# Kernel tuning notes

Measured on AMD Instinct MI355X. Metric: run time of the kernel, lower is better.

Reference implementation:

```python
import jax, jax.numpy as jnp
import numpy as np

V, E, H, W, S, T, B = 10000, 256, 512, 256, 512, 128, 64


def setup_inputs() -> dict:
    key = jax.random.key(0)
    ks = jax.random.split(key, 17)
    def rn(k, shape, s=0.08):
        return jax.random.normal(k, shape, jnp.float32) * s
    return {
        "tokens": jax.random.randint(ks[0], (B, S), 0, V),
        "dec_h0": jax.random.normal(ks[1], (B, H), jnp.float32),
        "emb_table": rn(ks[2], (V, E), 1.0),
        "enc_Wih": rn(ks[3], (4 * H, E)),
        "enc_Whh": rn(ks[4], (4 * H, H)),
        "enc_bih": rn(ks[5], (4 * H,)),
        "enc_bhh": rn(ks[6], (4 * H,)),
        "dec_Wih": rn(ks[7], (4 * H, E)),
        "dec_Whh": rn(ks[8], (4 * H, H)),
        "dec_bih": rn(ks[9], (4 * H,)),
        "dec_bhh": rn(ks[10], (4 * H,)),
        "W1_w": rn(ks[11], (W, H)),
        "W1_b": rn(ks[12], (W,)),
        "W2_w": rn(ks[13], (W, H)),
        "W2_b": rn(ks[14], (W,)),
        "vt_w": rn(ks[15], (1, W)),
        "vt_b": rn(ks[16], (1,)),
    }


def _lstm_cell(x, h, c, Wih, Whh, bih, bhh):
    # PyTorch gate order: input, forget, cell(g), output
    gates = x @ Wih.T + h @ Whh.T + bih + bhh
    i, f, g, o = jnp.split(gates, 4, axis=-1)
    c = jax.nn.sigmoid(f) * c + jax.nn.sigmoid(i) * jnp.tanh(g)
    h = jax.nn.sigmoid(o) * jnp.tanh(c)
    return h, c


def reference(tokens, dec_h0, emb_table, enc_Wih, enc_Whh, enc_bih, enc_bhh,
              dec_Wih, dec_Whh, dec_bih, dec_bhh, W1_w, W1_b, W2_w, W2_b,
              vt_w, vt_b):
    emb = emb_table[tokens]                       # [B,S,E]
    x_sbe = jnp.swapaxes(emb, 0, 1)               # [S,B,E] time-major
    bsz = tokens.shape[0]
    h0 = jnp.zeros((bsz, enc_Whh.shape[1]), emb.dtype)

    def enc_step(carry, x):
        h, c = carry
        h, c = _lstm_cell(x, h, c, enc_Wih, enc_Whh, enc_bih, enc_bhh)
        return (h, c), h

    _, enc_states = jax.lax.scan(enc_step, (h0, h0), x_sbe)   # [S,B,H]

    # W1(encoder_states) is constant across decoder steps -> hoist it
    blend1 = enc_states @ W1_w.T + W1_b            # [S,B,W]
    c0 = enc_states[-1]                            # original uses last enc state as cell init
    dec_in = jnp.zeros((bsz, emb_table.shape[1]), emb.dtype)  # never updated in original

    def dec_step(carry, _):
        h, c = carry
        h, c = _lstm_cell(dec_in, h, c, dec_Wih, dec_Whh, dec_bih, dec_bhh)
        blend2 = h @ W2_w.T + W2_b                 # [B,W]
        u = (jnp.tanh(blend1 + blend2[None]) @ vt_w.T)[..., 0] + vt_b[0]  # [S,B]
        logp = jax.nn.log_softmax(u.T, axis=1)     # [B,S], softmax over seq positions
        return (h, c), logp

    _, probs = jax.lax.scan(dec_step, (dec_h0, c0), None, length=T)  # [T,B,S]
    return jnp.swapaxes(probs, 0, 1)               # [B,T,S]
```

## Files before the change

kernel.cpp:

```cpp
#include <hip/hip_runtime.h>
#include <hip/hip_bf16.h>
#include <cstdint>
#include <cstddef>

typedef __bf16 bf16_t;
typedef __bf16 bf16x8 __attribute__((ext_vector_type(8)));
typedef float  f32x4  __attribute__((ext_vector_type(4)));

#define NB 64
#define NS 512
#define NTD 128
#define NE 256
#define NH 512
#define NG 2048
#define NW 256

#define HSTEP_DW 16384u

__device__ __forceinline__ float sigm_f(float x) { return 1.f / (1.f + __expf(-x)); }
__device__ __forceinline__ float tanh_f(float x) {
  float e = __expf(2.f * x);
  return 1.f - 2.f / (e + 1.f);
}
__device__ __forceinline__ float bits2f(uint32_t b16) {
  uint32_t u = b16 << 16;
  return __builtin_bit_cast(float, u);
}
__device__ __forceinline__ uint32_t packh(float a, float b) {
  uint16_t lo = __builtin_bit_cast(uint16_t, (bf16_t)a);
  uint16_t hi = __builtin_bit_cast(uint16_t, (bf16_t)b);
  return (uint32_t)lo | ((uint32_t)hi << 16);
}
__device__ __forceinline__ uint32_t aload(const uint32_t* p) {
  return __hip_atomic_load(p, __ATOMIC_RELAXED, __HIP_MEMORY_SCOPE_AGENT);
}
__device__ __forceinline__ uint64_t aload64(const uint64_t* p) {
  return __hip_atomic_load(p, __ATOMIC_RELAXED, __HIP_MEMORY_SCOPE_AGENT);
}
__device__ __forceinline__ void astore(uint32_t* p, uint32_t v) {
  __hip_atomic_store(p, v, __ATOMIC_RELAXED, __HIP_MEMORY_SCOPE_AGENT);
}

__global__ __launch_bounds__(256) void pack_all(
    const float* __restrict__ s0, bf16_t* __restrict__ d0,
    const float* __restrict__ s1, bf16_t* __restrict__ d1,
    const float* __restrict__ s2, bf16_t* __restrict__ d2,
    const float* __restrict__ s3, bf16_t* __restrict__ d3,
    const float* __restrict__ s4, bf16_t* __restrict__ d4) {
  int blk = blockIdx.x;
  const float* src; bf16_t* dst; int K, idx;
  if (blk < 2048)       { src = s0; dst = d0; K = 256; idx = blk * 256 + threadIdx.x; }
  else if (blk < 6144)  { src = s1; dst = d1; K = 512; idx = (blk - 2048) * 256 + threadIdx.x; }
  else if (blk < 10240) { src = s2; dst = d2; K = 512; idx = (blk - 6144) * 256 + threadIdx.x; }
  else if (blk < 10752) { src = s3; dst = d3; K = 512; idx = (blk - 10240) * 256 + threadIdx.x; }
  else                  { src = s4; dst = d4; K = 512; idx = (blk - 10752) * 256 + threadIdx.x; }
  int n = idx / K, k = idx - n * K;
  int lane = (((k & 31) >> 3) << 4) | (n & 15);
  size_t o = ((((size_t)(n >> 4) * (K >> 5)) + (k >> 5)) * 64 + lane) * 8 + (k & 7);
  dst[o] = (bf16_t)src[idx];
}

__global__ __launch_bounds__(256) void gather_emb2(
    const int* __restrict__ tokens, const float* __restrict__ table,
    bf16_t* __restrict__ embfrag, const float* __restrict__ dec_h0,
    uint32_t* __restrict__ dec_hf0) {
  int blk = blockIdx.x;
  if (blk < 4096) {
    int idx = blk * 256 + threadIdx.x;
    int row = idx >> 5, e0 = (idx & 31) << 3;
    int b = row & 63, s = row >> 6;
    int tok = tokens[b * NS + s];
    const float4* p = (const float4*)(table + (size_t)tok * NE + e0);
    float4 v0 = p[0], v1 = p[1];
    bf16x8 v;
    v[0] = (bf16_t)v0.x; v[1] = (bf16_t)v0.y; v[2] = (bf16_t)v0.z; v[3] = (bf16_t)v0.w;
    v[4] = (bf16_t)v1.x; v[5] = (bf16_t)v1.y; v[6] = (bf16_t)v1.z; v[7] = (bf16_t)v1.w;
    int mt = row >> 4;
    int ks = e0 >> 5;
    int lane = (b & 15) | (((e0 >> 3) & 3) << 4);
    *(bf16x8*)(embfrag + ((size_t)(mt * 8 + ks) * 64 + lane) * 8) = v;
  } else {
    int idx = (blk - 4096) * 256 + threadIdx.x;
    int b = idx >> 8, jp = idx & 255;
    int j = jp * 2;
    float lo = dec_h0[(size_t)b * NH + j], hi = dec_h0[(size_t)b * NH + j + 1];
    int bg = b >> 4, bl = b & 15, ks = j >> 5;
    int lane = bl | (((j >> 3) & 3) << 4);
    dec_hf0[((size_t)bg * 16 + ks) * 256 + lane * 4 + ((j >> 1) & 3)] = packh(lo, hi);
  }
}

__global__ __launch_bounds__(256) void gemm_blends(
    const bf16_t* __restrict__ encA, const bf16_t* __restrict__ W1p,
    const float* __restrict__ W1_b, bf16_t* __restrict__ blend1,
    const bf16_t* __restrict__ decA, const bf16_t* __restrict__ W2p,
    const float* __restrict__ W2_b, float* __restrict__ blend2) {
  union SMU { bf16_t t16[16][68]; float t32[16][68]; };
  __shared__ SMU tile;
  const int KS = 16;
  int lane = threadIdx.x & 63, w = threadIdx.x >> 6;
  int nt = blockIdx.x * 4 + w;
  bool is1 = blockIdx.y < 128;
  int mt0 = (is1 ? blockIdx.y : (blockIdx.y - 128)) * 16;
  const bf16_t* A  = is1 ? encA : decA;
  const bf16_t* Bp = is1 ? W1p : W2p;
  const float* bias = is1 ? W1_b : W2_b;
  bf16x8 bfr[KS];
  const bf16_t* bp = Bp + ((size_t)nt * KS * 64 + lane) * 8;
#pragma unroll
  for (int ks = 0; ks < KS; ++ks) bfr[ks] = *(const bf16x8*)(bp + (size_t)ks * 512);
  int col = (nt << 4) + (lane & 15);
  float bs = bias[col];
  int row0 = (lane >> 4) << 2;
  int rw = threadIdx.x >> 4, ch = threadIdx.x & 15;
  for (int m = 0; m < 16; ++m) {
    int mt = mt0 + m;
    const bf16_t* ap = A + (size_t)mt * (KS * 512) + lane * 8;
    f32x4 acc = {0.f, 0.f, 0.f, 0.f};
#pragma unroll
    for (int ks = 0; ks < KS; ++ks)
      acc = __builtin_amdgcn_mfma_f32_16x16x32_bf16(
          *(const bf16x8*)(ap + (size_t)ks * 512), bfr[ks], acc, 0, 0, 0);
    if (is1) {
#pragma unroll
      for (int r = 0; r < 4; ++r)
        tile.t16[row0 + r][w * 16 + (lane & 15)] = (bf16_t)(acc[r] + bs);
      __syncthreads();
      ushort4 v = *(const ushort4*)&tile.t16[rw][ch * 4];
      *(ushort4*)(blend1 + (size_t)(mt * 16 + rw) * NW + blockIdx.x * 64 + ch * 4) = v;
      __syncthreads();
    } else {
#pragma unroll
      for (int r = 0; r < 4; ++r)
        tile.t32[row0 + r][w * 16 + (lane & 15)] = acc[r] + bs;
      __syncthreads();
      float4 v = *(const float4*)&tile.t32[rw][ch * 4];
      *(float4*)(blend2 + (size_t)(mt * 16 + rw) * NW + blockIdx.x * 64 + ch * 4) = v;
      __syncthreads();
    }
  }
}

__global__ __launch_bounds__(256) void lstm_chain_enc(
    const bf16_t* __restrict__ Wp, const bf16_t* __restrict__ Wihp,
    const bf16_t* __restrict__ embfrag, const float* __restrict__ bih,
    const float* __restrict__ bhh, uint32_t* __restrict__ hfrag,
    uint32_t* __restrict__ flags) {
  __shared__ bf16_t wlds[8 * 8192];
  __shared__ float gl[4][16][36];
  int tid = threadIdx.x, lane = tid & 63, wv = tid >> 6;
  int bg = blockIdx.x >> 4, slice = blockIdx.x & 15;

  for (int l = 0; l < 8; ++l) {
    int g = l >> 1, p = l & 1;
    const bf16_t* src = Wp + (size_t)(g * 32 + slice * 2 + p) * 8192;
    bf16_t* dst = wlds + (size_t)l * 8192;
    for (int i = tid; i < 1024; i += 256)
      *(bf16x8*)(dst + (size_t)i * 8) = *(const bf16x8*)(src + (size_t)i * 8);
  }
  bf16x8 xf0[8], xf1[8];
  {
    int nt0 = wv * 32 + slice * 2;
    const bf16_t* p0 = Wihp + (((size_t)nt0 * 8) * 64 + lane) * 8;
    const bf16_t* p1 = Wihp + (((size_t)(nt0 + 1) * 8) * 64 + lane) * 8;
#pragma unroll
    for (int ks = 0; ks < 8; ++ks) {
      xf0[ks] = *(const bf16x8*)(p0 + (size_t)ks * 512);
      xf1[ks] = *(const bf16x8*)(p1 + (size_t)ks * 512);
    }
  }

  int ub = tid >> 4, uj2 = tid & 15;
  int j_lo = slice * 32 + uj2 * 2;
  int lane_f = ub | ((uj2 >> 2) << 4);
  float c0 = 0.f, c1 = 0.f;
  float bsum[4][2];
#pragma unroll
  for (int g = 0; g < 4; ++g) {
    bsum[g][0] = bih[g * NH + j_lo] + bhh[g * NH + j_lo];
    bsum[g][1] = bih[g * NH + j_lo + 1] + bhh[g * NH + j_lo + 1];
  }
  __syncthreads();

  const uint64_t* hq = (const uint64_t*)hfrag;
  uint32_t* fl = flags + bg * 16;

  for (int t = 0; t < NS; ++t) {
    bf16x8 ea[8];
    const bf16_t* eb = embfrag + (((size_t)(t * 4 + bg) * 8) * 64 + lane) * 8;
#pragma unroll
    for (int ks = 0; ks < 8; ++ks) ea[ks] = *(const bf16x8*)(eb + (size_t)ks * 512);
    if (t > 0) {
      uint32_t tgt = (uint32_t)t;
      bool ok;
      do {
        uint32_t f = tgt;
        if (lane < 16 && lane != (uint32_t)slice) f = aload(fl + lane);
        ok = __all(f >= tgt);
      } while (!ok);
    }
    f32x4 acc0 = {0.f, 0.f, 0.f, 0.f}, acc1 = {0.f, 0.f, 0.f, 0.f};
#pragma unroll
    for (int ks = 0; ks < 8; ++ks) {
      acc0 = __builtin_amdgcn_mfma_f32_16x16x32_bf16(ea[ks], xf0[ks], acc0, 0, 0, 0);
      acc1 = __builtin_amdgcn_mfma_f32_16x16x32_bf16(ea[ks], xf1[ks], acc1, 0, 0, 0);
    }
    const uint64_t* hb = hq + ((size_t)t * 4 + bg) * 2048 + lane * 2;
    uint64_t aq[16][2];
#pragma unroll
    for (int ks = 0; ks < 16; ++ks) {
      aq[ks][0] = aload64(hb + (size_t)ks * 128);
      aq[ks][1] = aload64(hb + (size_t)ks * 128 + 1);
    }
    const bf16_t* wl = wlds + (size_t)(wv * 2) * 8192 + lane * 8;
#pragma unroll
    for (int ks = 0; ks < 16; ++ks) {
      union { uint64_t q[2]; bf16x8 v; } u;
      u.q[0] = aq[ks][0]; u.q[1] = aq[ks][1];
      acc0 = __builtin_amdgcn_mfma_f32_16x16x32_bf16(
          u.v, *(const bf16x8*)(wl + (size_t)ks * 512), acc0, 0, 0, 0);
      acc1 = __builtin_amdgcn_mfma_f32_16x16x32_bf16(
          u.v, *(const bf16x8*)(wl + 8192 + (size_t)ks * 512), acc1, 0, 0, 0);
    }
    int cc = lane & 15, rb = (lane >> 4) << 2;
#pragma unroll
    for (int r = 0; r < 4; ++r) {
      gl[wv][rb + r][cc] = acc0[r];
      gl[wv][rb + r][16 + cc] = acc1[r];
    }
    __syncthreads();

    float p[4][2];
#pragma unroll
    for (int g = 0; g < 4; ++g) {
      p[g][0] = gl[g][ub][uj2 * 2] + bsum[g][0];
      p[g][1] = gl[g][ub][uj2 * 2 + 1] + bsum[g][1];
    }
    float i0 = sigm_f(p[0][0]), f0 = sigm_f(p[1][0]);
    float g0 = tanh_f(p[2][0]), o0 = sigm_f(p[3][0]);
    c0 = f0 * c0 + i0 * g0;
    float h0 = o0 * tanh_f(c0);
    float i1 = sigm_f(p[0][1]), f1 = sigm_f(p[1][1]);
    float g1 = tanh_f(p[2][1]), o1 = sigm_f(p[3][1]);
    c1 = f1 * c1 + i1 * g1;
    float h1 = o1 * tanh_f(c1);
    astore(hfrag + ((size_t)(t + 1) * 4 + bg) * 4096 +
               slice * 256 + lane_f * 4 + (uj2 & 3), packh(h0, h1));
    __syncthreads();
    if (tid == 0) astore(fl + slice, (uint32_t)(t + 1));
  }
}

__global__ __launch_bounds__(256) void lstm_chain_dec(
    const bf16_t* __restrict__ Wp, const float* __restrict__ bih,
    const float* __restrict__ bhh, uint32_t* __restrict__ hfrag,
    const uint32_t* __restrict__ c0frag, uint32_t* __restrict__ flags) {
  __shared__ bf16_t wlds[8 * 8192];
  __shared__ float gl[4][16][36];
  int tid = threadIdx.x, lane = tid & 63, wv = tid >> 6;
  int bg = blockIdx.x >> 4, slice = blockIdx.x & 15;

  for (int l = 0; l < 8; ++l) {
    int g = l >> 1, p = l & 1;
    const bf16_t* src = Wp + (size_t)(g * 32 + slice * 2 + p) * 8192;
    bf16_t* dst = wlds + (size_t)l * 8192;
    for (int i = tid; i < 1024; i += 256)
      *(bf16x8*)(dst + (size_t)i * 8) = *(const bf16x8*)(src + (size_t)i * 8);
  }
  int ub = tid >> 4, uj2 = tid & 15;
  int j_lo = slice * 32 + uj2 * 2;
  int lane_f = ub | ((uj2 >> 2) << 4);
  uint32_t d = c0frag[((size_t)bg * 16 + slice) * 256 + lane_f * 4 + (uj2 & 3)];
  float c0 = bits2f(d & 0xffffu), c1 = bits2f(d >> 16);
  float bsum[4][2];
#pragma unroll
  for (int g = 0; g < 4; ++g) {
    bsum[g][0] = bih[g * NH + j_lo] + bhh[g * NH + j_lo];
    bsum[g][1] = bih[g * NH + j_lo + 1] + bhh[g * NH + j_lo + 1];
  }
  __syncthreads();

  const uint64_t* hq = (const uint64_t*)hfrag;
  uint32_t* fl = flags + bg * 16;

  for (int t = 0; t < NTD; ++t) {
    if (t > 0) {
      uint32_t tgt = (uint32_t)t;
      bool ok;
      do {
        uint32_t f = tgt;
        if (lane < 16 && lane != (uint32_t)slice) f = aload(fl + lane);
        ok = __all(f >= tgt);
      } while (!ok);
    }
    const uint64_t* hb = hq + ((size_t)t * 4 + bg) * 2048 + lane * 2;
    uint64_t aq[16][2];
#pragma unroll
    for (int ks = 0; ks < 16; ++ks) {
      aq[ks][0] = aload64(hb + (size_t)ks * 128);
      aq[ks][1] = aload64(hb + (size_t)ks * 128 + 1);
    }
    const bf16_t* wl = wlds + (size_t)(wv * 2) * 8192 + lane * 8;
    f32x4 acc0 = {0.f, 0.f, 0.f, 0.f}, acc1 = {0.f, 0.f, 0.f, 0.f};
#pragma unroll
    for (int ks = 0; ks < 16; ++ks) {
      union { uint64_t q[2]; bf16x8 v; } u;
      u.q[0] = aq[ks][0]; u.q[1] = aq[ks][1];
      acc0 = __builtin_amdgcn_mfma_f32_16x16x32_bf16(
          u.v, *(const bf16x8*)(wl + (size_t)ks * 512), acc0, 0, 0, 0);
      acc1 = __builtin_amdgcn_mfma_f32_16x16x32_bf16(
          u.v, *(const bf16x8*)(wl + 8192 + (size_t)ks * 512), acc1, 0, 0, 0);
    }
    int cc = lane & 15, rb = (lane >> 4) << 2;
#pragma unroll
    for (int r = 0; r < 4; ++r) {
      gl[wv][rb + r][cc] = acc0[r];
      gl[wv][rb + r][16 + cc] = acc1[r];
    }
    __syncthreads();

    float p[4][2];
#pragma unroll
    for (int g = 0; g < 4; ++g) {
      p[g][0] = gl[g][ub][uj2 * 2] + bsum[g][0];
      p[g][1] = gl[g][ub][uj2 * 2 + 1] + bsum[g][1];
    }
    float i0 = sigm_f(p[0][0]), f0 = sigm_f(p[1][0]);
    float g0 = tanh_f(p[2][0]), o0 = sigm_f(p[3][0]);
    c0 = f0 * c0 + i0 * g0;
    float h0 = o0 * tanh_f(c0);
    float i1 = sigm_f(p[0][1]), f1 = sigm_f(p[1][1]);
    float g1 = tanh_f(p[2][1]), o1 = sigm_f(p[3][1]);
    c1 = f1 * c1 + i1 * g1;
    float h1 = o1 * tanh_f(c1);
    astore(hfrag + ((size_t)(t + 1) * 4 + bg) * 4096 +
               slice * 256 + lane_f * 4 + (uj2 & 3), packh(h0, h1));
    __syncthreads();
    if (tid == 0) astore(fl + slice, (uint32_t)(t + 1));
  }
}

__global__ __launch_bounds__(256) void attn_v2(const bf16_t* __restrict__ blend1,
                                               const float* __restrict__ blend2,
                                               const float* __restrict__ vt_w,
                                               float* __restrict__ out) {
  __shared__ float s_u[512], s_red[8];
  int t = blockIdx.x >> 6, b = blockIdx.x & 63;
  int tid = threadIdx.x, lane = tid & 63, wv = tid >> 6;
  int sslot = lane >> 4, wseg = lane & 15;
  int w0 = wseg * 16;

  float vt[16], b2[16];
  {
    const float4* vp = (const float4*)(vt_w + w0);
    const float4* bp = (const float4*)(blend2 + (size_t)(t * 64 + b) * NW + w0);
#pragma unroll
    for (int i = 0; i < 4; ++i) {
      float4 a = vp[i], c = bp[i];
      vt[i * 4 + 0] = a.x; vt[i * 4 + 1] = a.y; vt[i * 4 + 2] = a.z; vt[i * 4 + 3] = a.w;
      b2[i * 4 + 0] = c.x; b2[i * 4 + 1] = c.y; b2[i * 4 + 2] = c.z; b2[i * 4 + 3] = c.w;
    }
  }
  for (int p = 0; p < 32; ++p) {
    int s = p * 16 + wv * 4 + sslot;
    const bf16_t* row = blend1 + ((size_t)s * NB + b) * NW + w0;
    bf16x8 v0 = *(const bf16x8*)(row);
    bf16x8 v1 = *(const bf16x8*)(row + 8);
    float val = 0.f;
#pragma unroll
    for (int k = 0; k < 8; ++k) val += vt[k] * tanh_f((float)v0[k] + b2[k]);
#pragma unroll
    for (int k = 0; k < 8; ++k) val += vt[8 + k] * tanh_f((float)v1[k] + b2[8 + k]);
    val += __shfl_xor(val, 1, 64);
    val += __shfl_xor(val, 2, 64);
    val += __shfl_xor(val, 4, 64);
    val += __shfl_xor(val, 8, 64);
    if (wseg == 0) s_u[s] = val;
  }
  __syncthreads();
  float a = s_u[tid], bb2 = s_u[tid + 256];
  float m = fmaxf(a, bb2);
#pragma unroll
  for (int o = 1; o < 64; o <<= 1) m = fmaxf(m, __shfl_xor(m, o, 64));
  if (lane == 0) s_red[wv] = m;
  __syncthreads();
  m = fmaxf(fmaxf(s_red[0], s_red[1]), fmaxf(s_red[2], s_red[3]));
  float e = __expf(a - m) + __expf(bb2 - m);
#pragma unroll
  for (int o = 1; o < 64; o <<= 1) e += __shfl_xor(e, o, 64);
  if (lane == 0) s_red[4 + wv] = e;
  __syncthreads();
  float lz = m + logf(s_red[4] + s_red[5] + s_red[6] + s_red[7]);
  size_t ob = ((size_t)b * NTD + t) * NS;
  out[ob + tid] = a - lz;
  out[ob + tid + 256] = bb2 - lz;
}

extern "C" void kernel_launch(void* const* d_in, const int* in_sizes, int n_in,
                              void* d_out, int out_size, void* d_ws, size_t ws_size,
                              hipStream_t stream) {
  const int*   tokens    = (const int*)d_in[0];
  const float* dec_h0    = (const float*)d_in[1];
  const float* emb_table = (const float*)d_in[2];
  const float* enc_Wih   = (const float*)d_in[3];
  const float* enc_Whh   = (const float*)d_in[4];
  const float* enc_bih   = (const float*)d_in[5];
  const float* enc_bhh   = (const float*)d_in[6];
  const float* dec_Whh   = (const float*)d_in[8];
  const float* dec_bih   = (const float*)d_in[9];
  const float* dec_bhh   = (const float*)d_in[10];
  const float* W1_w      = (const float*)d_in[11];
  const float* W1_b      = (const float*)d_in[12];
  const float* W2_w      = (const float*)d_in[13];
  const float* W2_b      = (const float*)d_in[14];
  const float* vt_w      = (const float*)d_in[15];
  float* out = (float*)d_out;

  char* w = (char*)d_ws;
  size_t off = 0;
  auto alloc = [&](size_t bytes) {
    size_t o = off;
    off += (bytes + 255) & ~(size_t)255;
    return o;
  };
  bf16_t* embfrag = (bf16_t*)(w + alloc((size_t)NS * NB * NE * 2));
  uint32_t* enc_hf = (uint32_t*)(w + alloc((size_t)(NS + 1) * HSTEP_DW * 4));
  uint32_t* dec_hf = (uint32_t*)(w + alloc((size_t)(NTD + 1) * HSTEP_DW * 4));
  bf16_t* blend1  = (bf16_t*)(w + alloc((size_t)NS * NB * NW * 2));
  float*  blend2  = (float*)(w + alloc((size_t)NTD * NB * NW * 4));
  bf16_t* pWih    = (bf16_t*)(w + alloc((size_t)NG * NE * 2));
  bf16_t* pWhhE   = (bf16_t*)(w + alloc((size_t)NG * NH * 2));
  bf16_t* pWhhD   = (bf16_t*)(w + alloc((size_t)NG * NH * 2));
  bf16_t* pW1     = (bf16_t*)(w + alloc((size_t)NW * NH * 2));
  bf16_t* pW2     = (bf16_t*)(w + alloc((size_t)NW * NH * 2));
  uint32_t* flags = (uint32_t*)(w + alloc(512));
  (void)ws_size; (void)in_sizes; (void)n_in; (void)out_size;

  hipMemsetAsync(flags, 0, 512, stream);
  hipMemsetAsync(enc_hf, 0, HSTEP_DW * 4, stream);

  pack_all<<<11264, 256, 0, stream>>>(enc_Wih, pWih, enc_Whh, pWhhE,
                                      dec_Whh, pWhhD, W1_w, pW1, W2_w, pW2);

  gather_emb2<<<4160, 256, 0, stream>>>(tokens, emb_table, embfrag, dec_h0, dec_hf);

  lstm_chain_enc<<<64, 256, 0, stream>>>(pWhhE, pWih, embfrag,
                                         enc_bih, enc_bhh, enc_hf, flags);

  lstm_chain_dec<<<64, 256, 0, stream>>>(pWhhD, dec_bih, dec_bhh, dec_hf,
                                         enc_hf + (size_t)NS * HSTEP_DW,
                                         flags + 64);

  gemm_blends<<<dim3(4, 160), 256, 0, stream>>>(
      (const bf16_t*)(enc_hf + HSTEP_DW), pW1, W1_b, blend1,
      (const bf16_t*)(dec_hf + HSTEP_DW), pW2, W2_b, blend2);

  attn_v2<<<NTD * NB, 256, 0, stream>>>(blend1, blend2, vt_w, out);
}
```

Baseline: 2.668 ms.

## Split attention into LDS-tiled score kernel and separate log-softmax kernel

Attention scoring is restructured so that each block stages a 64-position chunk of blend1 for one batch into shared memory and reuses it across all 128 decoder steps. Before, every (t,b) block re-read the full blend1 slice from global memory. Raw scores now go to a new fp32 workspace buffer, and a second kernel applies log-softmax per row. This cuts repeated blend1 traffic but adds a 16 MB intermediate write and read plus one extra launch. Grid parallelism also drops to 512 blocks, each doing a long serial loop.

```diff
diff --git a/kernel.cpp b/kernel.cpp
--- a/kernel.cpp
+++ b/kernel.cpp
@@ -340,45 +340,73 @@
   }
 }
 
-__global__ __launch_bounds__(256) void attn_v2(const bf16_t* __restrict__ blend1,
-                                               const float* __restrict__ blend2,
-                                               const float* __restrict__ vt_w,
-                                               float* __restrict__ out) {
-  __shared__ float s_u[512], s_red[8];
-  int t = blockIdx.x >> 6, b = blockIdx.x & 63;
+__global__ __launch_bounds__(256) void attn_u(const bf16_t* __restrict__ blend1,
+                                              const float* __restrict__ blend2,
+                                              const float* __restrict__ vt_w,
+                                              float* __restrict__ u_out) {
+  __shared__ bf16_t b1[64 * 256];
+  int b = blockIdx.x >> 3, chunk = blockIdx.x & 7;
+  int s0 = chunk * 64;
   int tid = threadIdx.x, lane = tid & 63, wv = tid >> 6;
-  int sslot = lane >> 4, wseg = lane & 15;
+  int sslot = (lane >> 4), wseg = lane & 15;
   int w0 = wseg * 16;
 
-  float vt[16], b2[16];
+  {
+    int rr = tid >> 5, cc = (tid & 31) * 8;
+    for (int pass = 0; pass < 8; ++pass) {
+      int s = pass * 8 + rr;
+      bf16x8 v = *(const bf16x8*)(blend1 + ((size_t)(s0 + s) * NB + b) * NW + cc);
+      *(bf16x8*)(&b1[s * 256 + cc]) = v;
+    }
+  }
+  float vt[16];
   {
     const float4* vp = (const float4*)(vt_w + w0);
-    const float4* bp = (const float4*)(blend2 + (size_t)(t * 64 + b) * NW + w0);
 #pragma unroll
     for (int i = 0; i < 4; ++i) {
-      float4 a = vp[i], c = bp[i];
+      float4 a = vp[i];
       vt[i * 4 + 0] = a.x; vt[i * 4 + 1] = a.y; vt[i * 4 + 2] = a.z; vt[i * 4 + 3] = a.w;
-      b2[i * 4 + 0] = c.x; b2[i * 4 + 1] = c.y; b2[i * 4 + 2] = c.z; b2[i * 4 + 3] = c.w;
-    }
-  }
-  for (int p = 0; p < 32; ++p) {
-    int s = p * 16 + wv * 4 + sslot;
-    const bf16_t* row = blend1 + ((size_t)s * NB + b) * NW + w0;
-    bf16x8 v0 = *(const bf16x8*)(row);
-    bf16x8 v1 = *(const bf16x8*)(row + 8);
-    float val = 0.f;
-#pragma unroll
-    for (int k = 0; k < 8; ++k) val += vt[k] * tanh_f((float)v0[k] + b2[k]);
-#pragma unroll
-    for (int k = 0; k < 8; ++k) val += vt[8 + k] * tanh_f((float)v1[k] + b2[8 + k]);
-    val += __shfl_xor(val, 1, 64);
-    val += __shfl_xor(val, 2, 64);
-    val += __shfl_xor(val, 4, 64);
-    val += __shfl_xor(val, 8, 64);
-    if (wseg == 0) s_u[s] = val;
+    }
   }
   __syncthreads();
-  float a = s_u[tid], bb2 = s_u[tid + 256];
+
+  for (int pass = 0; pass < 8; ++pass) {
+    int t = pass * 16 + wv * 4 + sslot;
+    float b2[16];
+    {
+      const float4* bp = (const float4*)(blend2 + (size_t)(t * 64 + b) * NW + w0);
+#pragma unroll
+      for (int i = 0; i < 4; ++i) {
+        float4 c = bp[i];
+        b2[i * 4 + 0] = c.x; b2[i * 4 + 1] = c.y; b2[i * 4 + 2] = c.z; b2[i * 4 + 3] = c.w;
+      }
+    }
+    float* urow = u_out + ((size_t)b * NTD + t) * NS + s0;
+    for (int s = 0; s < 64; ++s) {
+      const bf16_t* row = &b1[s * 256 + w0];
+      bf16x8 v0 = *(const bf16x8*)(row);
+      bf16x8 v1 = *(const bf16x8*)(row + 8);
+      float val = 0.f;
+#pragma unroll
+      for (int k = 0; k < 8; ++k) val += vt[k] * tanh_f((float)v0[k] + b2[k]);
+#pragma unroll
+      for (int k = 0; k < 8; ++k) val += vt[8 + k] * tanh_f((float)v1[k] + b2[8 + k]);
+      val += __shfl_xor(val, 1, 64);
+      val += __shfl_xor(val, 2, 64);
+      val += __shfl_xor(val, 4, 64);
+      val += __shfl_xor(val, 8, 64);
+      if (wseg == 0) urow[s] = val;
+    }
+  }
+}
+
+__global__ __launch_bounds__(256) void logsm(const float* __restrict__ u_in,
+                                             float* __restrict__ out) {
+  __shared__ float s_red[8];
+  int row = blockIdx.x;
+  int tid = threadIdx.x, lane = tid & 63, wv = tid >> 6;
+  const float* ur = u_in + (size_t)row * NS;
+  float a = ur[tid], bb2 = ur[tid + 256];
   float m = fmaxf(a, bb2);
 #pragma unroll
   for (int o = 1; o < 64; o <<= 1) m = fmaxf(m, __shfl_xor(m, o, 64));
@@ -391,9 +419,9 @@
   if (lane == 0) s_red[4 + wv] = e;
   __syncthreads();
   float lz = m + logf(s_red[4] + s_red[5] + s_red[6] + s_red[7]);
-  size_t ob = ((size_t)b * NTD + t) * NS;
-  out[ob + tid] = a - lz;
-  out[ob + tid + 256] = bb2 - lz;
+  float* orow = out + (size_t)row * NS;
+  orow[tid] = a - lz;
+  orow[tid + 256] = bb2 - lz;
 }
 
 extern "C" void kernel_launch(void* const* d_in, const int* in_sizes, int n_in,
@@ -428,6 +456,7 @@
   uint32_t* dec_hf = (uint32_t*)(w + alloc((size_t)(NTD + 1) * HSTEP_DW * 4));
   bf16_t* blend1  = (bf16_t*)(w + alloc((size_t)NS * NB * NW * 2));
   float*  blend2  = (float*)(w + alloc((size_t)NTD * NB * NW * 4));
+  float*  ubuf    = (float*)(w + alloc((size_t)NB * NTD * NS * 4));
   bf16_t* pWih    = (bf16_t*)(w + alloc((size_t)NG * NE * 2));
   bf16_t* pWhhE   = (bf16_t*)(w + alloc((size_t)NG * NH * 2));
   bf16_t* pWhhD   = (bf16_t*)(w + alloc((size_t)NG * NH * 2));
@@ -455,5 +484,6 @@
       (const bf16_t*)(enc_hf + HSTEP_DW), pW1, W1_b, blend1,
       (const bf16_t*)(dec_hf + HSTEP_DW), pW2, W2_b, blend2);
 
-  attn_v2<<<NTD * NB, 256, 0, stream>>>(blend1, blend2, vt_w, out);
-}
+  attn_u<<<512, 256, 0, stream>>>(blend1, blend2, vt_w, ubuf);
+  logsm<<<NB * NTD, 256, 0, stream>>>(ubuf, out);
+}
```

Result: slower. 2.823 ms (+5.8%).
